# Performance work log

Measured on AMD Instinct MI355X. Metric: run time of the kernel, lower is better.

The kernel has to match this reference:

```python
import jax, jax.numpy as jnp
import numpy as np

N_EMB = 1024
EMB_DIM = 256
BETA = 0.25


def setup_inputs() -> dict:
    key = jax.random.key(0)
    k1, k2 = jax.random.split(key)
    z = jax.random.normal(k1, (32, EMB_DIM, 32, 32), dtype=jnp.float32)
    init = 1.0 / N_EMB
    emb = jax.random.uniform(k2, (N_EMB, EMB_DIM), dtype=jnp.float32,
                             minval=-init, maxval=init)
    return {"z": z, "emb": emb}


def reference(z, emb):
    # z: [B, C, H, W] -> [B, H, W, C]
    zc = jnp.transpose(z, (0, 2, 3, 1))
    z_flat = zc.reshape(-1, EMB_DIM)  # [N, D]

    # squared L2 distances: ||z||^2 + ||e||^2 - 2 z.e^T  -> [N, K]
    distances = (jnp.sum(z_flat ** 2, axis=1, keepdims=True)
                 + jnp.sum(emb ** 2, axis=1)
                 - 2.0 * (z_flat @ emb.T))
    nearest_idx = jnp.argmin(distances, axis=1)           # [N]
    nearest = jax.nn.one_hot(nearest_idx, N_EMB, dtype=jnp.float32)  # [N, K]

    # direct gather == one-hot matmul, same math
    zq = emb[nearest_idx].reshape(zc.shape)               # [B, H, W, C]

    loss = (jnp.mean((jax.lax.stop_gradient(zq) - zc) ** 2)
            + BETA * jnp.mean((zq - jax.lax.stop_gradient(zc)) ** 2))

    # straight-through estimator
    zq_st = zc + jax.lax.stop_gradient(zq - zc)

    e_mean = jnp.mean(nearest, axis=0)                    # [K]
    perplexity = jnp.exp(-jnp.sum(e_mean * jnp.log(e_mean + 1e-10)))

    zq_out = jnp.transpose(zq_st, (0, 3, 1, 2))           # back to NCHW
    return zq_out, loss, perplexity, nearest, nearest_idx[:, None]
```

## Files before the change

### kernel.cpp

```cpp
#include <hip/hip_runtime.h>

#define N_EMB  1024
#define EMB_D  256
#define HW     1024

#define OUT_ZQ      0
#define OUT_LOSS    8388608
#define OUT_PERP    8388609
#define OUT_NEAREST 8388610
#define OUT_IDX     41943042

#define WS_HIST   0
#define WS_ESQ    4096
#define WS_LOSSP  8192
#define WS_EH     12288
#define WS_TOTAL  536576

typedef unsigned long long ull;
typedef _Float16 half8 __attribute__((ext_vector_type(8)));
typedef float f32x4 __attribute__((ext_vector_type(4)));
typedef ull ull2 __attribute__((ext_vector_type(2)));

#define L_A     0
#define L_B     32768
#define L_ESQ   49152
#define L_ZSQ   53248
#define L_WIN   53504
#define L_RED   53760
#define L_TOT   55808

__device__ __forceinline__ void gload16(const void* g, void* l) {
    __builtin_amdgcn_global_load_lds(
        (const __attribute__((address_space(1))) unsigned int*)g,
        (__attribute__((address_space(3))) unsigned int*)l, 16, 0, 0);
}

__device__ __forceinline__ float pairwise8_combine(const float r[8]) {
    return __fadd_rn(__fadd_rn(__fadd_rn(r[0], r[1]), __fadd_rn(r[2], r[3])),
                     __fadd_rn(__fadd_rn(r[4], r[5]), __fadd_rn(r[6], r[7])));
}

__global__ void split_e(const float* __restrict__ emb, _Float16* __restrict__ eh) {
    int c = blockIdx.x;
    int k = threadIdx.x;
    eh[c * EMB_D + k] = (_Float16)emb[c * EMB_D + k];
}

__global__ void esq_kernel(const float* __restrict__ emb, float* __restrict__ esq,
                           int* __restrict__ hist) {
    int c = blockIdx.x * 256 + threadIdx.x;
    const float* p = emb + (size_t)c * EMB_D;
    float tot[2];
    #pragma unroll
    for (int h = 0; h < 2; ++h) {
        float r[8];
        #pragma unroll
        for (int i = 0; i < 8; ++i) {
            float x = p[h * 128 + i];
            r[i] = __fmul_rn(x, x);
        }
        for (int k = 8; k < 128; k += 8) {
            #pragma unroll
            for (int i = 0; i < 8; ++i) {
                float x = p[h * 128 + k + i];
                r[i] = __fadd_rn(r[i], __fmul_rn(x, x));
            }
        }
        tot[h] = pairwise8_combine(r);
    }
    esq[c] = __fadd_rn(tot[0], tot[1]);
    hist[c] = 0;
}

__global__ __launch_bounds__(256) void fused_vq(
        const float* __restrict__ z, const float* __restrict__ emb,
        const _Float16* __restrict__ eh, const float* __restrict__ esq,
        float* __restrict__ out, int* __restrict__ hist,
        double* __restrict__ lossp) {
    __shared__ __align__(16) char lds[L_TOT];
    int t = threadIdx.x, bid = blockIdx.x;
    int b = bid >> 4, hw0 = (bid & 15) << 6;
    int lane = t & 63, wave = t >> 6;
    int wm = wave >> 1, wn = wave & 1;
    int l15 = lane & 15, lq = lane >> 4;

    if (t >= 128) {
        int i = t - 128;
        #pragma unroll
        for (int q = 0; q < 8; ++q)
            *(float*)(lds + L_ESQ + (q * 128 + i) * 4) = esq[q * 128 + i];
    } else {
        int nl = t & 63, h = (t >> 6) & 1;
        const float* zp = z + ((size_t)b << 18) + hw0 + nl;
        int kb = h << 7;
        int abase = L_A + nl * 512;
        int sw = (nl & 7) << 4;
        float r[8];
        {   half8 hv;
            #pragma unroll
            for (int e = 0; e < 8; ++e) {
                float x = zp[(size_t)(kb + e) << 10];
                hv[e] = (_Float16)x;
                r[e] = __fmul_rn(x, x);
            }
            *(half8*)(lds + abase + (((kb << 1)) ^ sw)) = hv;
        }
        for (int c8 = 1; c8 < 16; ++c8) {
            half8 hv;
            #pragma unroll
            for (int e = 0; e < 8; ++e) {
                float x = zp[(size_t)(kb + c8 * 8 + e) << 10];
                hv[e] = (_Float16)x;
                r[e] = __fadd_rn(r[e], __fmul_rn(x, x));
            }
            *(half8*)(lds + abase + (((kb << 1) + c8 * 16) ^ sw)) = hv;
        }
        *(float*)(lds + L_RED + (h * 64 + nl) * 4) = pairwise8_combine(r);
    }
    __syncthreads();
    if (t < 64) {
        float t0 = *(float*)(lds + L_RED + t * 4);
        float t1 = *(float*)(lds + L_RED + 256 + t * 4);
        *(float*)(lds + L_ZSQ + t * 4) = __fadd_rn(t0, t1);
    }
    __syncthreads();

    int aoffs[2][2], boffs[4][2];
    #pragma unroll
    for (int i = 0; i < 2; ++i) {
        int r = wm * 32 + i * 16 + l15;
        #pragma unroll
        for (int kc = 0; kc < 2; ++kc)
            aoffs[i][kc] = L_A + r * 512 + ((kc * 64 + lq * 16) ^ ((r & 7) << 4));
    }
    #pragma unroll
    for (int j = 0; j < 4; ++j) {
        int c = wn * 64 + j * 16 + l15;
        #pragma unroll
        for (int kc = 0; kc < 2; ++kc)
            boffs[j][kc] = L_B + c * 128 + ((kc * 64 + lq * 16) ^ ((c & 7) << 4));
    }
    int bsrc[4], bdst[4];
    #pragma unroll
    for (int is = 0; is < 4; ++is) {
        int o = is * 4096 + t * 16;
        int col = o >> 7;
        int K = (o & 127) ^ ((col & 7) << 4);
        bsrc[is] = col * 256 + (K >> 1);
        bdst[is] = L_B + o;
    }
    float zs[8];
    #pragma unroll
    for (int s = 0; s < 8; ++s) {
        int row = wm * 32 + (s >> 2) * 16 + lq * 4 + (s & 3);
        zs[s] = *(const float*)(lds + L_ZSQ + row * 4);
    }
    ull k1[8], k2[8];
    #pragma unroll
    for (int s = 0; s < 8; ++s) { k1[s] = ~0ULL; k2[s] = ~0ULL; }

    for (int cbt = 0; cbt < 8; ++cbt) {
        f32x4 acc[2][4];
        #pragma unroll
        for (int i = 0; i < 2; ++i)
            #pragma unroll
            for (int j = 0; j < 4; ++j) acc[i][j] = (f32x4){0.f, 0.f, 0.f, 0.f};

        for (int kt = 0; kt < 4; ++kt) {
            __syncthreads();
            #pragma unroll
            for (int is = 0; is < 4; ++is)
                gload16(eh + cbt * 32768 + kt * 64 + bsrc[is], lds + bdst[is]);
            __syncthreads();

            half8 a[2][2], bb[4][2];
            #pragma unroll
            for (int i = 0; i < 2; ++i) {
                a[i][0] = *(const half8*)(lds + aoffs[i][0] + kt * 128);
                a[i][1] = *(const half8*)(lds + aoffs[i][1] + kt * 128);
            }
            #pragma unroll
            for (int j = 0; j < 4; ++j) {
                bb[j][0] = *(const half8*)(lds + boffs[j][0]);
                bb[j][1] = *(const half8*)(lds + boffs[j][1]);
            }
            #pragma unroll
            for (int i = 0; i < 2; ++i)
                #pragma unroll
                for (int j = 0; j < 4; ++j) {
                    acc[i][j] = __builtin_amdgcn_mfma_f32_16x16x32_f16(a[i][0], bb[j][0], acc[i][j], 0, 0, 0);
                    acc[i][j] = __builtin_amdgcn_mfma_f32_16x16x32_f16(a[i][1], bb[j][1], acc[i][j], 0, 0, 0);
                }
        }
        float es[4];
        #pragma unroll
        for (int j = 0; j < 4; ++j)
            es[j] = *(const float*)(lds + L_ESQ + ((cbt << 7) + wn * 64 + j * 16 + l15) * 4);
        #pragma unroll
        for (int i = 0; i < 2; ++i)
            #pragma unroll
            for (int r = 0; r < 4; ++r) {
                const int s = i * 4 + r;
                float zsv = zs[s];
                #pragma unroll
                for (int j = 0; j < 4; ++j) {
                    float d = __fsub_rn(__fadd_rn(zsv, es[j]), __fmul_rn(2.0f, acc[i][j][r]));
                    int cg = (cbt << 7) + wn * 64 + j * 16 + l15;
                    ull key = ((ull)__float_as_uint(d) << 32) | (unsigned)cg;
                    if (key < k1[s]) { k2[s] = k1[s]; k1[s] = key; }
                    else if (key < k2[s]) { k2[s] = key; }
                }
            }
    }

    __syncthreads();
    #pragma unroll
    for (int s = 0; s < 8; ++s) {
        int row = wm * 32 + (s >> 2) * 16 + lq * 4 + (s & 3);
        *(ull2*)(lds + L_A + row * 512 + ((wn << 4) + l15) * 16) = (ull2){k1[s], k2[s]};
    }
    __syncthreads();

    for (int rr = 0; rr < 16; ++rr) {
        int row = wave * 16 + rr;
        ull k = *(const ull*)(lds + L_A + row * 512 + lane * 8);
        ull kmin = k;
        #pragma unroll
        for (int m = 1; m < 64; m <<= 1) {
            ull o = __shfl_xor(kmin, m, 64);
            kmin = o < kmin ? o : kmin;
        }
        float dmin = __uint_as_float((unsigned)(kmin >> 32));
        float dme  = __uint_as_float((unsigned)(k >> 32));
        bool cand = dme <= __fadd_rn(dmin, 2e-4f);
        ull bal = __ballot(cand);
        int winner;
        if (__popcll(bal) == 1) {
            winner = (int)(unsigned)(kmin & 0xFFFFFFFFu);
        } else {
            const float* zp2 = z + ((size_t)b << 18) + hw0 + row;
            float zr[4];
            #pragma unroll
            for (int e = 0; e < 4; ++e) zr[e] = zp2[(size_t)(lane + 64 * e) << 10];
            float zsr = *(const float*)(lds + L_ZSQ + row * 4);
            ull bestk = ~0ULL;
            while (bal) {
                int src = __ffsll(bal) - 1;
                bal &= bal - 1;
                ull ck = __shfl(k, src, 64);
                int c = (int)(unsigned)(ck & 0xFFFFFFFFu);
                const float* ep = emb + (size_t)c * EMB_D;
                float p = __fmul_rn(zr[3], ep[lane + 192]);
                p = __builtin_fmaf(zr[2], ep[lane + 128], p);
                p = __builtin_fmaf(zr[1], ep[lane + 64], p);
                p = __builtin_fmaf(zr[0], ep[lane], p);
                #pragma unroll
                for (int m = 1; m < 64; m <<= 1)
                    p = __fadd_rn(p, __shfl_xor(p, m, 64));
                float ec = *(const float*)(lds + L_ESQ + c * 4);
                float d = __fsub_rn(__fadd_rn(zsr, ec), __fmul_rn(2.0f, p));
                ull kk = ((ull)__float_as_uint(d) << 32) | (unsigned)c;
                bestk = kk < bestk ? kk : bestk;
            }
            winner = (int)(unsigned)(bestk & 0xFFFFFFFFu);
        }
        size_t n = (size_t)bid * 64 + row;
        float* np = out + OUT_NEAREST + (n << 10);
        #pragma unroll
        for (int q = 0; q < 4; ++q) {
            int c4 = q * 256 + lane * 4;
            float4 v = { winner == c4     ? 1.f : 0.f, winner == c4 + 1 ? 1.f : 0.f,
                         winner == c4 + 2 ? 1.f : 0.f, winner == c4 + 3 ? 1.f : 0.f };
            *(float4*)(np + c4) = v;
        }
        if (lane == 0) {
            out[OUT_IDX + n] = (float)winner;
            atomicAdd(&hist[winner], 1);
            *(int*)(lds + L_WIN + row * 4) = winner;
        }
    }
    __syncthreads();

    {
        int hwl = t & 63, cq = t >> 6;
        int widx = *(const int*)(lds + L_WIN + hwl * 4);
        const float* zp3 = z + ((size_t)b << 18) + hw0 + hwl;
        float* oq = out + OUT_ZQ + ((size_t)b << 18) + hw0 + hwl;
        const float* er = emb + (size_t)widx * EMB_D;
        double s = 0.0;
        for (int cg = 0; cg < 16; ++cg) {
            int c0 = cq * 64 + cg * 4;
            float4 ev = *(const float4*)(er + c0);
            float evv[4] = {ev.x, ev.y, ev.z, ev.w};
            #pragma unroll
            for (int e = 0; e < 4; ++e) {
                size_t off = (size_t)(c0 + e) << 10;
                float zc = zp3[off];
                float diff = __fsub_rn(evv[e], zc);
                oq[off] = __fadd_rn(zc, diff);
                s += (double)__fmul_rn(diff, diff);
            }
        }
        *(double*)(lds + L_RED + t * 8) = s;
        __syncthreads();
        for (int st = 128; st > 0; st >>= 1) {
            if (t < st) {
                double o = *(double*)(lds + L_RED + (t + st) * 8);
                *(double*)(lds + L_RED + t * 8) += o;
            }
            __syncthreads();
        }
        if (t == 0) lossp[bid] = *(double*)(lds + L_RED);
    }
}

__global__ void finalize_scalars(const double* __restrict__ lossp,
                                 const int* __restrict__ hist,
                                 float* __restrict__ out_loss,
                                 float* __restrict__ out_perp) {
    __shared__ double sd[1024];
    int t = threadIdx.x;

    sd[t] = (t < 512) ? lossp[t] : 0.0;
    __syncthreads();
    for (int st = 512; st > 0; st >>= 1) {
        if (t < st) sd[t] += sd[t + st];
        __syncthreads();
    }
    if (t == 0) {
        double loss = 1.25 * (sd[0] / 8388608.0);
        *out_loss = (float)loss;
    }
    __syncthreads();

    float p = (float)hist[t] * (1.0f / 32768.0f);
    float term = __fmul_rn(p, logf(__fadd_rn(p, 1e-10f)));
    sd[t] = (double)term;
    __syncthreads();
    for (int st = 512; st > 0; st >>= 1) {
        if (t < st) sd[t] += sd[t + st];
        __syncthreads();
    }
    if (t == 0) *out_perp = expf(-(float)sd[0]);
}

extern "C" void kernel_launch(void* const* d_in, const int* in_sizes, int n_in,
                              void* d_out, int out_size, void* d_ws, size_t ws_size,
                              hipStream_t stream) {
    const float* z   = (const float*)d_in[0];
    const float* emb = (const float*)d_in[1];
    float* out = (float*)d_out;
    char*  ws  = (char*)d_ws;

    int*      hist  = (int*)(ws + WS_HIST);
    float*    esq   = (float*)(ws + WS_ESQ);
    double*   lossp = (double*)(ws + WS_LOSSP);
    _Float16* eh    = (_Float16*)(ws + WS_EH);

    esq_kernel<<<N_EMB / 256, 256, 0, stream>>>(emb, esq, hist);
    split_e<<<N_EMB, 256, 0, stream>>>(emb, eh);

    fused_vq<<<512, 256, 0, stream>>>(z, emb, eh, esq, out, hist, lossp);

    finalize_scalars<<<1, 1024, 0, stream>>>(lossp, hist,
                                             out + OUT_LOSS, out + OUT_PERP);
}
```

Baseline: 85.77 us.

## Overlap one-hot zero fill with GEMM loop, merge prep kernels, vectorize epilogue

The 128MB one-hot output is now zero-filled in chunks inside the distance GEMM loop, interleaved with the LDS tile loads, and each row's single 1.0 is written by one lane afterwards. This hides the large store stream behind the MFMA work instead of writing it serially at the end. The two preprocessing kernels are merged into one launch, the esq load into LDS uses vector loads, and the zq/loss epilogue now uses float4 accesses along the spatial dimension. The risk is that the zero-fill stores compete with the GEMM for memory bandwidth, and correctness relies on the zero store landing before the 1.0 store, which barriers in the same block should guarantee.

```diff
diff --git a/kernel.cpp b/kernel.cpp
--- a/kernel.cpp
+++ b/kernel.cpp
@@ -13,8 +13,8 @@
 #define WS_HIST   0
 #define WS_ESQ    4096
 #define WS_LOSSP  8192
-#define WS_EH     12288
-#define WS_TOTAL  536576
+#define WS_EH     16384
+#define WS_TOTAL  540672
 
 typedef unsigned long long ull;
 typedef _Float16 half8 __attribute__((ext_vector_type(8)));
@@ -40,15 +40,15 @@
                      __fadd_rn(__fadd_rn(r[4], r[5]), __fadd_rn(r[6], r[7])));
 }
 
-__global__ void split_e(const float* __restrict__ emb, _Float16* __restrict__ eh) {
-    int c = blockIdx.x;
-    int k = threadIdx.x;
-    eh[c * EMB_D + k] = (_Float16)emb[c * EMB_D + k];
-}
-
-__global__ void esq_kernel(const float* __restrict__ emb, float* __restrict__ esq,
-                           int* __restrict__ hist) {
-    int c = blockIdx.x * 256 + threadIdx.x;
+__global__ void prep(const float* __restrict__ emb, _Float16* __restrict__ eh,
+                     float* __restrict__ esq, int* __restrict__ hist) {
+    int bid = blockIdx.x;
+    if (bid < 1024) {
+        int c = bid, k = threadIdx.x;
+        eh[c * EMB_D + k] = (_Float16)emb[c * EMB_D + k];
+        return;
+    }
+    int c = (bid - 1024) * 256 + threadIdx.x;
     const float* p = emb + (size_t)c * EMB_D;
     float tot[2];
     #pragma unroll
@@ -87,8 +87,10 @@
     if (t >= 128) {
         int i = t - 128;
         #pragma unroll
-        for (int q = 0; q < 8; ++q)
-            *(float*)(lds + L_ESQ + (q * 128 + i) * 4) = esq[q * 128 + i];
+        for (int q = 0; q < 2; ++q) {
+            f32x4 v = *(const f32x4*)(esq + (q * 128 + i) * 4);
+            *(f32x4*)(lds + L_ESQ + (q * 128 + i) * 16) = v;
+        }
     } else {
         int nl = t & 63, h = (t >> 6) & 1;
         const float* zp = z + ((size_t)b << 18) + hw0 + nl;
@@ -159,6 +161,9 @@
     #pragma unroll
     for (int s = 0; s < 8; ++s) { k1[s] = ~0ULL; k2[s] = ~0ULL; }
 
+    float* nbase = out + OUT_NEAREST + (((size_t)bid * 64) << 10);
+    const f32x4 zzero = {0.f, 0.f, 0.f, 0.f};
+
     for (int cbt = 0; cbt < 8; ++cbt) {
         f32x4 acc[2][4];
         #pragma unroll
@@ -167,10 +172,16 @@
             for (int j = 0; j < 4; ++j) acc[i][j] = (f32x4){0.f, 0.f, 0.f, 0.f};
 
         for (int kt = 0; kt < 4; ++kt) {
+            const int r = cbt * 4 + kt;
             __syncthreads();
             #pragma unroll
             for (int is = 0; is < 4; ++is)
                 gload16(eh + cbt * 32768 + kt * 64 + bsrc[is], lds + bdst[is]);
+            {
+                float* zp0 = nbase + (((size_t)(2 * r + (t >> 7))) << 10) + (t & 127) * 8;
+                *(f32x4*)zp0 = zzero;
+                *(f32x4*)(zp0 + 4) = zzero;
+            }
             __syncthreads();
 
             half8 a[2][2], bb[4][2];
@@ -265,15 +276,8 @@
             winner = (int)(unsigned)(bestk & 0xFFFFFFFFu);
         }
         size_t n = (size_t)bid * 64 + row;
-        float* np = out + OUT_NEAREST + (n << 10);
-        #pragma unroll
-        for (int q = 0; q < 4; ++q) {
-            int c4 = q * 256 + lane * 4;
-            float4 v = { winner == c4     ? 1.f : 0.f, winner == c4 + 1 ? 1.f : 0.f,
-                         winner == c4 + 2 ? 1.f : 0.f, winner == c4 + 3 ? 1.f : 0.f };
-            *(float4*)(np + c4) = v;
-        }
         if (lane == 0) {
+            out[OUT_NEAREST + (n << 10) + winner] = 1.0f;
             out[OUT_IDX + n] = (float)winner;
             atomicAdd(&hist[winner], 1);
             *(int*)(lds + L_WIN + row * 4) = winner;
@@ -282,24 +286,24 @@
     __syncthreads();
 
     {
-        int hwl = t & 63, cq = t >> 6;
-        int widx = *(const int*)(lds + L_WIN + hwl * 4);
-        const float* zp3 = z + ((size_t)b << 18) + hw0 + hwl;
-        float* oq = out + OUT_ZQ + ((size_t)b << 18) + hw0 + hwl;
-        const float* er = emb + (size_t)widx * EMB_D;
+        int q = t & 15;
+        int cq = t >> 4;
+        int4 w4 = *(const int4*)(lds + L_WIN + q * 16);
+        const float* zb = z + ((size_t)b << 18) + hw0 + q * 4;
+        float* ob = out + OUT_ZQ + ((size_t)b << 18) + hw0 + q * 4;
         double s = 0.0;
-        for (int cg = 0; cg < 16; ++cg) {
-            int c0 = cq * 64 + cg * 4;
-            float4 ev = *(const float4*)(er + c0);
-            float evv[4] = {ev.x, ev.y, ev.z, ev.w};
-            #pragma unroll
-            for (int e = 0; e < 4; ++e) {
-                size_t off = (size_t)(c0 + e) << 10;
-                float zc = zp3[off];
-                float diff = __fsub_rn(evv[e], zc);
-                oq[off] = __fadd_rn(zc, diff);
-                s += (double)__fmul_rn(diff, diff);
-            }
+        for (int i = 0; i < 16; ++i) {
+            int c = cq + (i << 4);
+            f32x4 zc = *(const f32x4*)(zb + ((size_t)c << 10));
+            f32x4 ev = { emb[(size_t)w4.x * EMB_D + c], emb[(size_t)w4.y * EMB_D + c],
+                         emb[(size_t)w4.z * EMB_D + c], emb[(size_t)w4.w * EMB_D + c] };
+            f32x4 df = { __fsub_rn(ev[0], zc[0]), __fsub_rn(ev[1], zc[1]),
+                         __fsub_rn(ev[2], zc[2]), __fsub_rn(ev[3], zc[3]) };
+            f32x4 st = { __fadd_rn(zc[0], df[0]), __fadd_rn(zc[1], df[1]),
+                         __fadd_rn(zc[2], df[2]), __fadd_rn(zc[3], df[3]) };
+            *(f32x4*)(ob + ((size_t)c << 10)) = st;
+            s += (double)__fmul_rn(df[0], df[0]) + (double)__fmul_rn(df[1], df[1])
+               + (double)__fmul_rn(df[2], df[2]) + (double)__fmul_rn(df[3], df[3]);
         }
         *(double*)(lds + L_RED + t * 8) = s;
         __syncthreads();
@@ -357,11 +361,8 @@
     double*   lossp = (double*)(ws + WS_LOSSP);
     _Float16* eh    = (_Float16*)(ws + WS_EH);
 
-    esq_kernel<<<N_EMB / 256, 256, 0, stream>>>(emb, esq, hist);
-    split_e<<<N_EMB, 256, 0, stream>>>(emb, eh);
-
+    prep<<<1028, 256, 0, stream>>>(emb, eh, esq, hist);
     fused_vq<<<512, 256, 0, stream>>>(z, emb, eh, esq, out, hist, lossp);
-
     finalize_scalars<<<1, 1024, 0, stream>>>(lossp, hist,
                                              out + OUT_LOSS, out + OUT_PERP);
 }
```

Result: slower. 88.82 us (+3.6%).
